# Kernel tuning notes

Hardware: AMD Instinct MI355X
Metric: run time of the kernel (lower is better)

## Reference

```python
import jax, jax.numpy as jnp
import numpy as np
import math

H = 12
DH = 64
MAX_POS = 1024

def setup_inputs() -> dict:
    key = jax.random.key(0)
    ks = jax.random.split(key, 8)
    B, L, D = 2, 1024, 768
    s = 0.02
    return {
        "hidden_states": jax.random.normal(ks[0], (B, L, D), jnp.float32),
        "attention_mask": jnp.zeros((B, 1, 1, L), jnp.float32),
        "struct_matrix": jax.random.uniform(ks[1], (5, B, 1, L, L), jnp.float32),
        "Wq": jax.random.normal(ks[2], (D, D), jnp.float32) * s,
        "bq": jnp.zeros((D,), jnp.float32),
        "Wk": jax.random.normal(ks[3], (D, D), jnp.float32) * s,
        "bk": jnp.zeros((D,), jnp.float32),
        "Wv": jax.random.normal(ks[4], (D, D), jnp.float32) * s,
        "bv": jnp.zeros((D,), jnp.float32),
        "dist_emb": jax.random.normal(ks[5], (2 * MAX_POS - 1, DH), jnp.float32) * s,
        "ssan_w": jax.random.normal(ks[6], (5, H, DH, DH), jnp.float32) * s,
        "abs_bias": jnp.zeros((5, H), jnp.float32),
    }

def reference(hidden_states, attention_mask, struct_matrix, Wq, bq, Wk, bk, Wv, bv, dist_emb, ssan_w, abs_bias):
    B, L, D = hidden_states.shape

    def heads(x):  # [B,L,D] -> [B,H,L,dh]
        return x.reshape(B, L, H, DH).transpose(0, 2, 1, 3)

    q = heads(hidden_states @ Wq + bq)
    k = heads(hidden_states @ Wk + bk)
    v = heads(hidden_states @ Wv + bv)

    scores = jnp.einsum('bhqd,bhkd->bhqk', q, k)

    # relative_key_query positional scores
    pos_ids = jnp.arange(L)
    distance = pos_ids[:, None] - pos_ids[None, :]          # [L,L]
    pos = dist_emb[distance + MAX_POS - 1]                  # [L,L,dh]
    scores = scores + jnp.einsum('bhld,lrd->bhlr', q, pos)
    scores = scores + jnp.einsum('bhrd,lrd->bhlr', k, pos)

    scores = scores / math.sqrt(DH)
    scores = scores + attention_mask

    # 5 SSAN bilinear bias terms, masked by structural matrices
    for i in range(5):
        bias = jnp.einsum('bhqd,hde,bhke->bhqk', q, ssan_w[i], k)
        scores = scores + (bias + abs_bias[i][None, :, None, None]) * struct_matrix[i]

    probs = jax.nn.softmax(scores, axis=-1)
    ctx = jnp.einsum('bhqk,bhkd->bqhd', probs, v).reshape(B, L, D)
    return ctx
```

## Files before the change

kernel.cpp:

```cpp
#include <hip/hip_runtime.h>
#include <math.h>

#define NB 2
#define NL 1024
#define ND 768
#define NH 12
#define DH 64

typedef _Float16 f16;
typedef _Float16 f16x4 __attribute__((ext_vector_type(4)));
typedef _Float16 f16x8 __attribute__((ext_vector_type(8)));
typedef float f32x4 __attribute__((ext_vector_type(4)));

#define MFMA16(a, b, c) __builtin_amdgcn_mfma_f32_16x16x32_f16((a), (b), (c), 0, 0, 0)

__device__ __forceinline__ void soft_barrier() {
    asm volatile("s_waitcnt lgkmcnt(0)\n\ts_barrier" ::: "memory");
}

__global__ __launch_bounds__(256) void prep_kernel(
    const float* __restrict__ hs,
    const float* __restrict__ Wq, const float* __restrict__ Wk,
    const float* __restrict__ Wv, const float* __restrict__ sw,
    const float* __restrict__ de,
    f16* __restrict__ hsf, f16* __restrict__ wt, f16* __restrict__ swt,
    f16* __restrict__ de16)
{
    __shared__ float sT[64 * 66];
    const int t = threadIdx.x;
    const int tile = blockIdx.x;

    if (tile < 768) {
        const int base = tile * 2048 + t * 8;
        float4 a = *(const float4*)&hs[base];
        float4 b = *(const float4*)&hs[base + 4];
        f16x8 hv;
        hv[0] = (f16)a.x; hv[1] = (f16)a.y; hv[2] = (f16)a.z; hv[3] = (f16)a.w;
        hv[4] = (f16)b.x; hv[5] = (f16)b.y; hv[6] = (f16)b.z; hv[7] = (f16)b.w;
        *(f16x8*)&hsf[base] = hv;
        return;
    }
    if (tile >= 1260) {
        const int base = (tile - 1260) * 2048 + t * 8;
        if (base < 2047 * 64) {
            float4 a = *(const float4*)&de[base];
            float4 b = *(const float4*)&de[base + 4];
            f16x8 hv;
            hv[0] = (f16)a.x; hv[1] = (f16)a.y; hv[2] = (f16)a.z; hv[3] = (f16)a.w;
            hv[4] = (f16)b.x; hv[5] = (f16)b.y; hv[6] = (f16)b.z; hv[7] = (f16)b.w;
            *(f16x8*)&de16[base] = hv;
        }
        return;
    }

    const float* S; f16* D; int sRS, dRS;
    const int ti = tile - 768;
    if (ti < 432) {
        const int mat = ti / 144, r2 = ti % 144, ht = r2 / 12, kt = r2 % 12;
        const float* W = (mat == 0) ? Wq : (mat == 1) ? Wk : Wv;
        S = W + (size_t)(kt * 64) * ND + ht * 64;
        D = wt + (size_t)((mat * NH + ht) * 64) * ND + kt * 64;
        sRS = ND; dRS = ND;
    } else {
        const int i = ti - 432;
        S = sw + (size_t)i * 4096;
        D = swt + (size_t)i * 4096;
        sRS = 64; dRS = 64;
    }

    {
        const int kk = t >> 2, nb = (t & 3) * 16;
        float v[16];
        #pragma unroll
        for (int j = 0; j < 4; ++j)
            *(float4*)&v[4 * j] = *(const float4*)&S[(size_t)kk * sRS + nb + 4 * j];
        #pragma unroll
        for (int jj = 0; jj < 16; ++jj)
            sT[(nb + jj) * 66 + kk] = v[jj];
    }
    soft_barrier();
    {
        const int n = t >> 2, kb = (t & 3) * 16;
        f16 tmp[16];
        #pragma unroll
        for (int j = 0; j < 8; ++j) {
            float2 x = *(float2*)&sT[n * 66 + kb + 2 * j];
            tmp[2 * j]     = (f16)x.x;
            tmp[2 * j + 1] = (f16)x.y;
        }
        *(f16x8*)&D[(size_t)n * dRS + kb]     = *(f16x8*)&tmp[0];
        *(f16x8*)&D[(size_t)n * dRS + kb + 8] = *(f16x8*)&tmp[8];
    }
}

__global__ __launch_bounds__(256, 4) void qkv_kernel(
    const f16* __restrict__ hsf, const f16* __restrict__ wt,
    const float* __restrict__ bq, const float* __restrict__ bk,
    const float* __restrict__ bv,
    f16* __restrict__ qf, f16* __restrict__ kf, f16* __restrict__ vt)
{
    __shared__ f16 sA[64 * 72], sB[64 * 72];
    __shared__ float sT[64 * 66];

    const int m0  = blockIdx.x * 64;
    const int y   = blockIdx.y;
    const int mat = y / NH, h = y % NH;
    const int t = threadIdx.x, lane = t & 63, w = t >> 6;
    const int quad = lane >> 4, l15 = lane & 15;
    const int wm = w >> 1, wn = w & 1;

    const float* bias = (mat == 0) ? bq : (mat == 1) ? bk : bv;

    f32x4 acc[2][2];
    #pragma unroll
    for (int r = 0; r < 2; ++r)
        #pragma unroll
        for (int c = 0; c < 2; ++c) acc[r][c] = (f32x4){0.f, 0.f, 0.f, 0.f};

    const int srow = t >> 2, scol = (t & 3) * 16;
    const f16* Ag = hsf + (size_t)(m0 + srow) * ND + scol;
    const f16* Bg = wt + ((size_t)y * 64 + srow) * ND + scol;

    for (int k0 = 0; k0 < ND; k0 += 64) {
        soft_barrier();
        *(f16x8*)&sA[srow * 72 + scol]     = *(const f16x8*)&Ag[k0];
        *(f16x8*)&sA[srow * 72 + scol + 8] = *(const f16x8*)&Ag[k0 + 8];
        *(f16x8*)&sB[srow * 72 + scol]     = *(const f16x8*)&Bg[k0];
        *(f16x8*)&sB[srow * 72 + scol + 8] = *(const f16x8*)&Bg[k0 + 8];
        soft_barrier();
        #pragma unroll
        for (int kk = 0; kk < 64; kk += 32) {
            const int ko = kk + quad * 8;
            f16x8 a0 = *(f16x8*)&sA[(32 * wm + l15) * 72 + ko];
            f16x8 a1 = *(f16x8*)&sA[(32 * wm + 16 + l15) * 72 + ko];
            f16x8 b0 = *(f16x8*)&sB[(32 * wn + l15) * 72 + ko];
            f16x8 b1 = *(f16x8*)&sB[(32 * wn + 16 + l15) * 72 + ko];
            acc[0][0] = MFMA16(a0, b0, acc[0][0]);
            acc[0][1] = MFMA16(a0, b1, acc[0][1]);
            acc[1][0] = MFMA16(a1, b0, acc[1][0]);
            acc[1][1] = MFMA16(a1, b1, acc[1][1]);
        }
    }
    soft_barrier();

    const int bb = m0 >> 10;
    const int lbase = m0 & 1023;
    const int bh = bb * NH + h;

    if (mat < 2) {
        #pragma unroll
        for (int r = 0; r < 2; ++r)
            #pragma unroll
            for (int c = 0; c < 2; ++c) {
                const int col = 32 * wn + 16 * c + l15;
                const float bz = bias[h * 64 + col];
                #pragma unroll
                for (int rr = 0; rr < 4; ++rr)
                    sT[(32 * wm + 16 * r + 4 * quad + rr) * 66 + col] = acc[r][c][rr] + bz;
            }
        soft_barrier();
        const int orow = t >> 2, ocb = (t & 3) * 16;
        f16 tmp[16];
        #pragma unroll
        for (int j = 0; j < 8; ++j) {
            float2 x = *(float2*)&sT[orow * 66 + ocb + 2 * j];
            tmp[2 * j] = (f16)x.x; tmp[2 * j + 1] = (f16)x.y;
        }
        f16* dst = ((mat == 0) ? qf : kf) + ((size_t)bh * NL + lbase + orow) * DH + ocb;
        *(f16x8*)dst       = *(f16x8*)&tmp[0];
        *(f16x8*)(dst + 8) = *(f16x8*)&tmp[8];
    } else {
        #pragma unroll
        for (int r = 0; r < 2; ++r)
            #pragma unroll
            for (int c = 0; c < 2; ++c) {
                const int col = 32 * wn + 16 * c + l15;
                const float bz = bias[h * 64 + col];
                #pragma unroll
                for (int rr = 0; rr < 4; ++rr)
                    sT[col * 66 + 32 * wm + 16 * r + 4 * quad + rr] = acc[r][c][rr] + bz;
            }
        soft_barrier();
        const int d = t >> 2, lcb = (t & 3) * 16;
        f16 tmp[16];
        #pragma unroll
        for (int j = 0; j < 8; ++j) {
            float2 x = *(float2*)&sT[d * 66 + lcb + 2 * j];
            tmp[2 * j] = (f16)x.x; tmp[2 * j + 1] = (f16)x.y;
        }
        f16* dst = vt + ((size_t)bh * DH + d) * NL + lbase + lcb;
        *(f16x8*)dst       = *(f16x8*)&tmp[0];
        *(f16x8*)(dst + 8) = *(f16x8*)&tmp[8];
    }
}

__global__ __launch_bounds__(256, 4) void qw_kernel(
    const f16* __restrict__ qf, const f16* __restrict__ swt,
    f16* __restrict__ qwf)
{
    __shared__ f16 sA[64 * 72], sB[64 * 72];
    __shared__ float sT[64 * 66];

    const int l0 = blockIdx.x * 64;
    const int z  = blockIdx.y;
    const int p  = z / 24, bh = z % 24, h = bh % NH;
    const int t = threadIdx.x, lane = t & 63, w = t >> 6;
    const int quad = lane >> 4, l15 = lane & 15;
    const int wm = w >> 1, wn = w & 1;

    const int srow = t >> 2, scol = (t & 3) * 16;
    {
        const f16* As = qf + ((size_t)bh * NL + l0 + srow) * DH + scol;
        const f16* Bs = swt + ((size_t)(p * NH + h) * 64 + srow) * 64 + scol;
        *(f16x8*)&sA[srow * 72 + scol]     = *(const f16x8*)As;
        *(f16x8*)&sA[srow * 72 + scol + 8] = *(const f16x8*)(As + 8);
        *(f16x8*)&sB[srow * 72 + scol]     = *(const f16x8*)Bs;
        *(f16x8*)&sB[srow * 72 + scol + 8] = *(const f16x8*)(Bs + 8);
    }
    soft_barrier();

    f32x4 acc[2][2];
    #pragma unroll
    for (int r = 0; r < 2; ++r)
        #pragma unroll
        for (int c = 0; c < 2; ++c) acc[r][c] = (f32x4){0.f, 0.f, 0.f, 0.f};

    #pragma unroll
    for (int kk = 0; kk < 64; kk += 32) {
        const int ko = kk + quad * 8;
        f16x8 a0 = *(f16x8*)&sA[(32 * wm + l15) * 72 + ko];
        f16x8 a1 = *(f16x8*)&sA[(32 * wm + 16 + l15) * 72 + ko];
        f16x8 b0 = *(f16x8*)&sB[(32 * wn + l15) * 72 + ko];
        f16x8 b1 = *(f16x8*)&sB[(32 * wn + 16 + l15) * 72 + ko];
        acc[0][0] = MFMA16(a0, b0, acc[0][0]);
        acc[0][1] = MFMA16(a0, b1, acc[0][1]);
        acc[1][0] = MFMA16(a1, b0, acc[1][0]);
        acc[1][1] = MFMA16(a1, b1, acc[1][1]);
    }
    soft_barrier();

    #pragma unroll
    for (int r = 0; r < 2; ++r)
        #pragma unroll
        for (int c = 0; c < 2; ++c) {
            const int col = 32 * wn + 16 * c + l15;
            #pragma unroll
            for (int rr = 0; rr < 4; ++rr)
                sT[(32 * wm + 16 * r + 4 * quad + rr) * 66 + col] = acc[r][c][rr];
        }
    soft_barrier();

    const int orow = t >> 2, ocb = (t & 3) * 16;
    f16 tmp[16];
    #pragma unroll
    for (int j = 0; j < 8; ++j) {
        float2 x = *(float2*)&sT[orow * 66 + ocb + 2 * j];
        tmp[2 * j] = (f16)x.x; tmp[2 * j + 1] = (f16)x.y;
    }
    f16* dst = qwf + ((size_t)(p * 24 + bh) * NL + l0 + orow) * DH + ocb;
    *(f16x8*)dst       = *(f16x8*)&tmp[0];
    *(f16x8*)(dst + 8) = *(f16x8*)&tmp[8];
}

__global__ __launch_bounds__(256, 2) void attn_kernel(
    const f16* __restrict__ qf, const f16* __restrict__ kf,
    const f16* __restrict__ vt, const f16* __restrict__ qwf,
    const float* __restrict__ mask, const float* __restrict__ struct_m,
    const f16* __restrict__ de16, const float* __restrict__ abs_bias,
    float* __restrict__ out)
{
    __shared__ f16 sK[64 * 72];
    __shared__ f16 sVt[2][64 * 72];
    __shared__ f16 sE[96 * 72];
    __shared__ f16 sQEl[96 * 34];
    __shared__ f16 sKEl[96 * 66];
    __shared__ float sS[32 * 68];
    __shared__ f16 sP[32 * 72];
    __shared__ float sAlpha[32], sL[32];

    const int l0 = blockIdx.x * 32;
    const int bh = blockIdx.y;
    const int bb = bh / NH, h = bh % NH;
    const int t  = threadIdx.x;
    const int lane  = t & 63;
    const int w     = t >> 6;
    const int quad  = lane >> 4;
    const int l15   = lane & 15;
    const int msub  = w >> 1;
    const int npair = w & 1;

    const size_t NQKV = (size_t)NB * NH * NL * DH;

    f16x8 aQ[2], aW[5][2];
    {
        const size_t qrow = ((size_t)bh * NL + l0 + 16 * msub + l15) * DH;
        #pragma unroll
        for (int K = 0; K < 2; ++K) {
            aQ[K] = *(const f16x8*)&qf[qrow + 32 * K + 8 * quad];
            #pragma unroll
            for (int p = 0; p < 5; ++p)
                aW[p][K] = *(const f16x8*)&qwf[p * NQKV + qrow + 32 * K + 8 * quad];
        }
    }

    float ab[5];
    #pragma unroll
    for (int p = 0; p < 5; ++p) ab[p] = abs_bias[p * NH + h];

    float pf_st[5][2][4], pf_mask[2];

    auto stage_kv = [&](int r0s, int buf) {
        const int row = t >> 3, col = (t & 7) * 8;
        const f16* ks = kf + ((size_t)bh * NL + r0s) * DH;
        *(f16x8*)&sK[row * 72 + col]        = *(const f16x8*)&ks[row * 64 + col];
        *(f16x8*)&sK[(row + 32) * 72 + col] = *(const f16x8*)&ks[(row + 32) * 64 + col];
        const f16* vs = vt + (size_t)bh * DH * NL + r0s;
        *(f16x8*)&sVt[buf][row * 72 + col] =
            *(const f16x8*)&vs[(size_t)row * NL + col];
        *(f16x8*)&sVt[buf][(row + 32) * 72 + col] =
            *(const f16x8*)&vs[(size_t)(row + 32) * NL + col];
    };

    auto stage_E = [&](int r0s) {
        const int ebase = l0 - r0s + 960;
        #pragma unroll
        for (int p = 0; p < 3; ++p) {
            const int idx = t + 256 * p;
            const int er = idx >> 3, col = (idx & 7) * 8;
            if (er < 95)
                *(f16x8*)&sE[er * 72 + col] =
                    *(const f16x8*)&de16[(size_t)(ebase + er) * DH + col];
        }
    };

    auto prefetch = [&](int r0s) {
        #pragma unroll
        for (int n = 0; n < 2; ++n) {
            const int j = 32 * npair + 16 * n + l15;
            pf_mask[n] = mask[bb * NL + r0s + j];
            #pragma unroll
            for (int r = 0; r < 4; ++r) {
                const int i = 16 * msub + 4 * quad + r;
                #pragma unroll
                for (int p = 0; p < 5; ++p)
                    pf_st[p][n][r] =
                        struct_m[((size_t)(p * NB + bb) * NL + l0 + i) * NL + r0s + j];
            }
        }
    };

    stage_kv(0, 0);
    stage_E(0);
    prefetch(0);

    const int sm_i = t >> 3;
    const int sm_jb = t & 7;
    float m_cur = -INFINITY, l_cur = 0.f;
    f32x4 O[2];
    O[0] = (f32x4){0.f, 0.f, 0.f, 0.f};
    O[1] = (f32x4){0.f, 0.f, 0.f, 0.f};

    for (int kt = 0; kt < 16; ++kt) {
        const int cur = kt & 1;
        soft_barrier();

        {
            f16x8 ak0 = *(f16x8*)&sK[(16 * w + l15) * 72 + quad * 8];
            f16x8 ak1 = *(f16x8*)&sK[(16 * w + l15) * 72 + 32 + quad * 8];
            #pragma unroll
            for (int c = 0; c < 3; ++c) {
                const int nt = 3 * npair + c;
                f16x8 e0 = *(f16x8*)&sE[(16 * nt + l15) * 72 + quad * 8];
                f16x8 e1 = *(f16x8*)&sE[(16 * nt + l15) * 72 + 32 + quad * 8];
                f32x4 cq = {0.f, 0.f, 0.f, 0.f};
                cq = MFMA16(aQ[0], e0, cq);
                cq = MFMA16(aQ[1], e1, cq);
                #pragma unroll
                for (int r = 0; r < 4; ++r)
                    sQEl[(16 * nt + l15) * 34 + 16 * msub + 4 * quad + r] = (f16)cq[r];
            }
            #pragma unroll
            for (int nt = 0; nt < 6; ++nt) {
                f16x8 e0 = *(f16x8*)&sE[(16 * nt + l15) * 72 + quad * 8];
                f16x8 e1 = *(f16x8*)&sE[(16 * nt + l15) * 72 + 32 + quad * 8];
                f32x4 ck = {0.f, 0.f, 0.f, 0.f};
                ck = MFMA16(ak0, e0, ck);
                ck = MFMA16(ak1, e1, ck);
                #pragma unroll
                for (int r = 0; r < 4; ++r)
                    sKEl[(16 * nt + l15) * 66 + 16 * w + 4 * quad + r] = (f16)ck[r];
            }
        }
        soft_barrier();

        {
            f32x4 acc[2][6];
            #pragma unroll
            for (int n = 0; n < 2; ++n)
                #pragma unroll
                for (int p = 0; p < 6; ++p)
                    acc[n][p] = (f32x4){0.f, 0.f, 0.f, 0.f};

            #pragma unroll
            for (int K = 0; K < 2; ++K) {
                const int koff = K * 32 + quad * 8;
                f16x8 bk2[2];
                #pragma unroll
                for (int n = 0; n < 2; ++n)
                    bk2[n] = *(f16x8*)&sK[(32 * npair + 16 * n + l15) * 72 + koff];
                #pragma unroll
                for (int n = 0; n < 2; ++n)
                    acc[n][0] = MFMA16(aQ[K], bk2[n], acc[n][0]);
                #pragma unroll
                for (int p = 0; p < 5; ++p)
                    #pragma unroll
                    for (int n = 0; n < 2; ++n)
                        acc[n][1 + p] = MFMA16(aW[p][K], bk2[n], acc[n][1 + p]);
            }

            #pragma unroll
            for (int n = 0; n < 2; ++n) {
                const int j = 32 * npair + 16 * n + l15;
                #pragma unroll
                for (int r = 0; r < 4; ++r) {
                    const int i = 16 * msub + 4 * quad + r;
                    const int tp = i - j + 63;
                    float posv = (float)sQEl[tp * 34 + i] + (float)sKEl[tp * 66 + j];
                    float s = (acc[n][0][r] + posv) * 0.125f + pf_mask[n];
                    #pragma unroll
                    for (int p = 0; p < 5; ++p)
                        s += (acc[n][1 + p][r] + ab[p]) * pf_st[p][n][r];
                    sS[i * 68 + j] = s;
                }
            }
        }
        soft_barrier();

        {
            float sv[8];
            float smax = -INFINITY;
            #pragma unroll
            for (int k = 0; k < 8; ++k) {
                sv[k] = sS[sm_i * 68 + sm_jb + 8 * k];
                smax = fmaxf(smax, sv[k]);
            }
            #pragma unroll
            for (int off = 4; off > 0; off >>= 1)
                smax = fmaxf(smax, __shfl_xor(smax, off, 8));
            const float m_new = fmaxf(m_cur, smax);
            const float alpha = __expf(m_cur - m_new);
            float rsum = 0.f;
            #pragma unroll
            for (int k = 0; k < 8; ++k) {
                float p = __expf(sv[k] - m_new);
                sP[sm_i * 72 + sm_jb + 8 * k] = (f16)p;
                rsum += p;
            }
            #pragma unroll
            for (int off = 4; off > 0; off >>= 1)
                rsum += __shfl_xor(rsum, off, 8);
            l_cur = l_cur * alpha + rsum;
            m_cur = m_new;
            if (sm_jb == 0) { sAlpha[sm_i] = alpha; sL[sm_i] = l_cur; }
        }
        soft_barrier();

        {
            if (kt < 15) {
                stage_kv((kt + 1) * 64, cur ^ 1);
                stage_E((kt + 1) * 64);
                prefetch((kt + 1) * 64);
            }

            float a4[4];
            #pragma unroll
            for (int r = 0; r < 4; ++r) a4[r] = sAlpha[16 * msub + 4 * quad + r];
            #pragma unroll
            for (int n = 0; n < 2; ++n)
                #pragma unroll
                for (int r = 0; r < 4; ++r) O[n][r] *= a4[r];

            const int prow = (16 * msub + l15) * 72;
            #pragma unroll
            for (int K = 0; K < 2; ++K) {
                const int koff = K * 32 + quad * 8;
                f16x8 pfr = *(f16x8*)&sP[prow + koff];
                #pragma unroll
                for (int n = 0; n < 2; ++n) {
                    f16x8 vfr = *(f16x8*)&sVt[cur][(32 * npair + 16 * n + l15) * 72 + koff];
                    O[n] = MFMA16(pfr, vfr, O[n]);
                }
            }
        }
    }

    float linv[4];
    #pragma unroll
    for (int r = 0; r < 4; ++r) linv[r] = 1.0f / sL[16 * msub + 4 * quad + r];
    #pragma unroll
    for (int n = 0; n < 2; ++n) {
        const int dh = 32 * npair + 16 * n + l15;
        #pragma unroll
        for (int r = 0; r < 4; ++r) {
            const int i = 16 * msub + 4 * quad + r;
            out[((size_t)bb * NL + l0 + i) * ND + h * DH + dh] = O[n][r] * linv[r];
        }
    }
}

extern "C" void kernel_launch(void* const* d_in, const int* in_sizes, int n_in,
                              void* d_out, int out_size, void* d_ws, size_t ws_size,
                              hipStream_t stream) {
    const float* hs   = (const float*)d_in[0];
    const float* mask = (const float*)d_in[1];
    const float* stm  = (const float*)d_in[2];
    const float* Wq   = (const float*)d_in[3];
    const float* bq   = (const float*)d_in[4];
    const float* Wk   = (const float*)d_in[5];
    const float* bk   = (const float*)d_in[6];
    const float* Wv   = (const float*)d_in[7];
    const float* bv   = (const float*)d_in[8];
    const float* de   = (const float*)d_in[9];
    const float* sw   = (const float*)d_in[10];
    const float* abb  = (const float*)d_in[11];
    float* outp = (float*)d_out;

    const size_t NQKV = (size_t)NB * NH * NL * DH;
    char* ws = (char*)d_ws;
    f16* qf   = (f16*)ws;                 ws += NQKV * 2;
    f16* kf   = (f16*)ws;                 ws += NQKV * 2;
    f16* vtb  = (f16*)ws;                 ws += NQKV * 2;
    f16* qwf  = (f16*)ws;                 ws += 5 * NQKV * 2;
    f16* hsf  = (f16*)ws;                 ws += NQKV * 2;
    f16* wt   = (f16*)ws;                 ws += (size_t)2304 * 768 * 2;
    f16* swt  = (f16*)ws;                 ws += (size_t)245760 * 2;
    f16* de16 = (f16*)ws;

    prep_kernel<<<1324, 256, 0, stream>>>(hs, Wq, Wk, Wv, sw, de,
                                          hsf, wt, swt, de16);
    qkv_kernel<<<dim3(32, 36), 256, 0, stream>>>(hsf, wt, bq, bk, bv, qf, kf, vtb);
    qw_kernel<<<dim3(16, 120), 256, 0, stream>>>(qf, swt, qwf);
    attn_kernel<<<dim3(32, 24), 256, 0, stream>>>(qf, kf, vtb, qwf,
                                                  mask, stm, de16, abb, outp);
}
```

Before: 243.2 us.

## Fold SSAN weights into Q projection and widen attention to 512 threads

Precomputes Wq·ssan_w[i] per head, plus the matching projected bias, in a new small kernel. The five qW projections then come directly from hidden_states inside one merged projection GEMM, which removes the separate qw kernel and its serial dependency on q. The attention kernel moves from 256 to 512 threads, with each wave owning one 16-column tile, and the relative-position Q/K·E products are redistributed across all waves with a reshaped shared layout. The qW GEMM now has a K dimension of 768 instead of 64, so it does more FLOPs, and the product is folded in fp16, which may change accuracy slightly.

```diff
diff --git a/kernel.cpp b/kernel.cpp
--- a/kernel.cpp
+++ b/kernel.cpp
@@ -21,10 +21,8 @@
 __global__ __launch_bounds__(256) void prep_kernel(
     const float* __restrict__ hs,
     const float* __restrict__ Wq, const float* __restrict__ Wk,
-    const float* __restrict__ Wv, const float* __restrict__ sw,
-    const float* __restrict__ de,
-    f16* __restrict__ hsf, f16* __restrict__ wt, f16* __restrict__ swt,
-    f16* __restrict__ de16)
+    const float* __restrict__ Wv, const float* __restrict__ de,
+    f16* __restrict__ hsf, f16* __restrict__ wt, f16* __restrict__ de16)
 {
     __shared__ float sT[64 * 66];
     const int t = threadIdx.x;
@@ -40,8 +38,8 @@
         *(f16x8*)&hsf[base] = hv;
         return;
     }
-    if (tile >= 1260) {
-        const int base = (tile - 1260) * 2048 + t * 8;
+    if (tile >= 1200) {
+        const int base = (tile - 1200) * 2048 + t * 8;
         if (base < 2047 * 64) {
             float4 a = *(const float4*)&de[base];
             float4 b = *(const float4*)&de[base + 4];
@@ -53,27 +51,18 @@
         return;
     }
 
-    const float* S; f16* D; int sRS, dRS;
     const int ti = tile - 768;
-    if (ti < 432) {
-        const int mat = ti / 144, r2 = ti % 144, ht = r2 / 12, kt = r2 % 12;
-        const float* W = (mat == 0) ? Wq : (mat == 1) ? Wk : Wv;
-        S = W + (size_t)(kt * 64) * ND + ht * 64;
-        D = wt + (size_t)((mat * NH + ht) * 64) * ND + kt * 64;
-        sRS = ND; dRS = ND;
-    } else {
-        const int i = ti - 432;
-        S = sw + (size_t)i * 4096;
-        D = swt + (size_t)i * 4096;
-        sRS = 64; dRS = 64;
-    }
+    const int mat = ti / 144, r2 = ti % 144, ht = r2 / 12, kt = r2 % 12;
+    const float* W = (mat == 0) ? Wq : (mat == 1) ? Wk : Wv;
+    const float* S = W + (size_t)(kt * 64) * ND + ht * 64;
+    f16* D = wt + (size_t)((mat * NH + ht) * 64) * ND + kt * 64;
 
     {
         const int kk = t >> 2, nb = (t & 3) * 16;
         float v[16];
         #pragma unroll
         for (int j = 0; j < 4; ++j)
-            *(float4*)&v[4 * j] = *(const float4*)&S[(size_t)kk * sRS + nb + 4 * j];
+            *(float4*)&v[4 * j] = *(const float4*)&S[(size_t)kk * ND + nb + 4 * j];
         #pragma unroll
         for (int jj = 0; jj < 16; ++jj)
             sT[(nb + jj) * 66 + kk] = v[jj];
@@ -88,23 +77,102 @@
             tmp[2 * j]     = (f16)x.x;
             tmp[2 * j + 1] = (f16)x.y;
         }
-        *(f16x8*)&D[(size_t)n * dRS + kb]     = *(f16x8*)&tmp[0];
-        *(f16x8*)&D[(size_t)n * dRS + kb + 8] = *(f16x8*)&tmp[8];
+        *(f16x8*)&D[(size_t)n * ND + kb]     = *(f16x8*)&tmp[0];
+        *(f16x8*)&D[(size_t)n * ND + kb + 8] = *(f16x8*)&tmp[8];
     }
 }
 
-__global__ __launch_bounds__(256, 4) void qkv_kernel(
+__global__ __launch_bounds__(256, 2) void wq5_kernel(
+    const float* __restrict__ Wq, const float* __restrict__ bq,
+    const float* __restrict__ sw,
+    f16* __restrict__ wq5t, float* __restrict__ bq5)
+{
+    __shared__ float sAT[64 * 69];
+    __shared__ float sB[64 * 64];
+    __shared__ float sT[64 * 66];
+
+    const int ktile = blockIdx.x;
+    const int z  = blockIdx.y;
+    const int h  = z % NH;
+    const int k0 = ktile * 64;
+    const int t  = threadIdx.x;
+
+    {
+        const int kk = t >> 2, db = (t & 3) * 16;
+        float v[16];
+        #pragma unroll
+        for (int j = 0; j < 4; ++j)
+            *(float4*)&v[4 * j] = *(const float4*)&Wq[(size_t)(k0 + kk) * ND + h * 64 + db + 4 * j];
+        #pragma unroll
+        for (int jj = 0; jj < 16; ++jj)
+            sAT[(db + jj) * 69 + kk] = v[jj];
+        #pragma unroll
+        for (int j = 0; j < 4; ++j)
+            *(float4*)&sB[16 * t + 4 * j] = *(const float4*)&sw[(size_t)z * 4096 + 16 * t + 4 * j];
+    }
+    soft_barrier();
+
+    const int tr = t >> 4, tc = t & 15;
+    float acc[4][4];
+    #pragma unroll
+    for (int r = 0; r < 4; ++r)
+        #pragma unroll
+        for (int c = 0; c < 4; ++c) acc[r][c] = 0.f;
+
+    #pragma unroll 8
+    for (int d = 0; d < 64; ++d) {
+        float a[4], b[4];
+        *(float4*)a = *(const float4*)&sAT[d * 69 + tr * 4];
+        *(float4*)b = *(const float4*)&sB[d * 64 + tc * 4];
+        #pragma unroll
+        for (int r = 0; r < 4; ++r)
+            #pragma unroll
+            for (int c = 0; c < 4; ++c)
+                acc[r][c] += a[r] * b[c];
+    }
+
+    if (ktile == 0 && t < 64) {
+        float s = 0.f;
+        for (int d = 0; d < 64; ++d) s += bq[h * 64 + d] * sB[d * 64 + t];
+        bq5[z * 64 + t] = s;
+    }
+
+    #pragma unroll
+    for (int r = 0; r < 4; ++r)
+        #pragma unroll
+        for (int c = 0; c < 4; ++c)
+            sT[(tc * 4 + c) * 66 + tr * 4 + r] = acc[r][c];
+    soft_barrier();
+
+    const int e = t >> 2, kb = (t & 3) * 16;
+    f16 tmp[16];
+    #pragma unroll
+    for (int j = 0; j < 8; ++j) {
+        float2 x = *(float2*)&sT[e * 66 + kb + 2 * j];
+        tmp[2 * j] = (f16)x.x; tmp[2 * j + 1] = (f16)x.y;
+    }
+    f16* dst = wq5t + ((size_t)z * 64 + e) * ND + k0 + kb;
+    *(f16x8*)dst       = *(f16x8*)&tmp[0];
+    *(f16x8*)(dst + 8) = *(f16x8*)&tmp[8];
+}
+
+__global__ __launch_bounds__(256, 4) void proj_kernel(
     const f16* __restrict__ hsf, const f16* __restrict__ wt,
+    const f16* __restrict__ wq5t, const float* __restrict__ bq5,
     const float* __restrict__ bq, const float* __restrict__ bk,
     const float* __restrict__ bv,
-    f16* __restrict__ qf, f16* __restrict__ kf, f16* __restrict__ vt)
+    f16* __restrict__ qf, f16* __restrict__ kf, f16* __restrict__ vt,
+    f16* __restrict__ qwf)
 {
     __shared__ f16 sA[64 * 72], sB[64 * 72];
     __shared__ float sT[64 * 66];
 
     const int m0  = blockIdx.x * 64;
     const int y   = blockIdx.y;
-    const int mat = y / NH, h = y % NH;
+    const bool isqw = (y >= 36);
+    const int mat = isqw ? 3 : y / NH;
+    const int z2  = isqw ? (y - 36) : 0;
+    const int h   = isqw ? (z2 % NH) : (y % NH);
     const int t = threadIdx.x, lane = t & 63, w = t >> 6;
     const int quad = lane >> 4, l15 = lane & 15;
     const int wm = w >> 1, wn = w & 1;
@@ -119,7 +187,8 @@
 
     const int srow = t >> 2, scol = (t & 3) * 16;
     const f16* Ag = hsf + (size_t)(m0 + srow) * ND + scol;
-    const f16* Bg = wt + ((size_t)y * 64 + srow) * ND + scol;
+    const f16* Bg = (isqw ? wq5t + (size_t)z2 * 64 * ND : wt + (size_t)y * 64 * ND)
+                    + (size_t)srow * ND + scol;
 
     for (int k0 = 0; k0 < ND; k0 += 64) {
         soft_barrier();
@@ -147,29 +216,7 @@
     const int lbase = m0 & 1023;
     const int bh = bb * NH + h;
 
-    if (mat < 2) {
-        #pragma unroll
-        for (int r = 0; r < 2; ++r)
-            #pragma unroll
-            for (int c = 0; c < 2; ++c) {
-                const int col = 32 * wn + 16 * c + l15;
-                const float bz = bias[h * 64 + col];
-                #pragma unroll
-                for (int rr = 0; rr < 4; ++rr)
-                    sT[(32 * wm + 16 * r + 4 * quad + rr) * 66 + col] = acc[r][c][rr] + bz;
-            }
-        soft_barrier();
-        const int orow = t >> 2, ocb = (t & 3) * 16;
-        f16 tmp[16];
-        #pragma unroll
-        for (int j = 0; j < 8; ++j) {
-            float2 x = *(float2*)&sT[orow * 66 + ocb + 2 * j];
-            tmp[2 * j] = (f16)x.x; tmp[2 * j + 1] = (f16)x.y;
-        }
-        f16* dst = ((mat == 0) ? qf : kf) + ((size_t)bh * NL + lbase + orow) * DH + ocb;
-        *(f16x8*)dst       = *(f16x8*)&tmp[0];
-        *(f16x8*)(dst + 8) = *(f16x8*)&tmp[8];
-    } else {
+    if (mat == 2) {
         #pragma unroll
         for (int r = 0; r < 2; ++r)
             #pragma unroll
@@ -191,89 +238,50 @@
         f16* dst = vt + ((size_t)bh * DH + d) * NL + lbase + lcb;
         *(f16x8*)dst       = *(f16x8*)&tmp[0];
         *(f16x8*)(dst + 8) = *(f16x8*)&tmp[8];
+    } else {
+        #pragma unroll
+        for (int r = 0; r < 2; ++r)
+            #pragma unroll
+            for (int c = 0; c < 2; ++c) {
+                const int col = 32 * wn + 16 * c + l15;
+                const float bz = isqw ? bq5[z2 * 64 + col] : bias[h * 64 + col];
+                #pragma unroll
+                for (int rr = 0; rr < 4; ++rr)
+                    sT[(32 * wm + 16 * r + 4 * quad + rr) * 66 + col] = acc[r][c][rr] + bz;
+            }
+        soft_barrier();
+        const int orow = t >> 2, ocb = (t & 3) * 16;
+        f16 tmp[16];
+        #pragma unroll
+        for (int j = 0; j < 8; ++j) {
+            float2 x = *(float2*)&sT[orow * 66 + ocb + 2 * j];
+            tmp[2 * j] = (f16)x.x; tmp[2 * j + 1] = (f16)x.y;
+        }
+        f16* dst;
+        if (isqw) {
+            const int p = z2 / NH;
+            dst = qwf + ((size_t)(p * 24 + bh) * NL + lbase + orow) * DH + ocb;
+        } else {
+            dst = ((mat == 0) ? qf : kf) + ((size_t)bh * NL + lbase + orow) * DH + ocb;
+        }
+        *(f16x8*)dst       = *(f16x8*)&tmp[0];
+        *(f16x8*)(dst + 8) = *(f16x8*)&tmp[8];
     }
 }
 
-__global__ __launch_bounds__(256, 4) void qw_kernel(
-    const f16* __restrict__ qf, const f16* __restrict__ swt,
-    f16* __restrict__ qwf)
-{
-    __shared__ f16 sA[64 * 72], sB[64 * 72];
-    __shared__ float sT[64 * 66];
-
-    const int l0 = blockIdx.x * 64;
-    const int z  = blockIdx.y;
-    const int p  = z / 24, bh = z % 24, h = bh % NH;
-    const int t = threadIdx.x, lane = t & 63, w = t >> 6;
-    const int quad = lane >> 4, l15 = lane & 15;
-    const int wm = w >> 1, wn = w & 1;
-
-    const int srow = t >> 2, scol = (t & 3) * 16;
-    {
-        const f16* As = qf + ((size_t)bh * NL + l0 + srow) * DH + scol;
-        const f16* Bs = swt + ((size_t)(p * NH + h) * 64 + srow) * 64 + scol;
-        *(f16x8*)&sA[srow * 72 + scol]     = *(const f16x8*)As;
-        *(f16x8*)&sA[srow * 72 + scol + 8] = *(const f16x8*)(As + 8);
-        *(f16x8*)&sB[srow * 72 + scol]     = *(const f16x8*)Bs;
-        *(f16x8*)&sB[srow * 72 + scol + 8] = *(const f16x8*)(Bs + 8);
-    }
-    soft_barrier();
-
-    f32x4 acc[2][2];
-    #pragma unroll
-    for (int r = 0; r < 2; ++r)
-        #pragma unroll
-        for (int c = 0; c < 2; ++c) acc[r][c] = (f32x4){0.f, 0.f, 0.f, 0.f};
-
-    #pragma unroll
-    for (int kk = 0; kk < 64; kk += 32) {
-        const int ko = kk + quad * 8;
-        f16x8 a0 = *(f16x8*)&sA[(32 * wm + l15) * 72 + ko];
-        f16x8 a1 = *(f16x8*)&sA[(32 * wm + 16 + l15) * 72 + ko];
-        f16x8 b0 = *(f16x8*)&sB[(32 * wn + l15) * 72 + ko];
-        f16x8 b1 = *(f16x8*)&sB[(32 * wn + 16 + l15) * 72 + ko];
-        acc[0][0] = MFMA16(a0, b0, acc[0][0]);
-        acc[0][1] = MFMA16(a0, b1, acc[0][1]);
-        acc[1][0] = MFMA16(a1, b0, acc[1][0]);
-        acc[1][1] = MFMA16(a1, b1, acc[1][1]);
-    }
-    soft_barrier();
-
-    #pragma unroll
-    for (int r = 0; r < 2; ++r)
-        #pragma unroll
-        for (int c = 0; c < 2; ++c) {
-            const int col = 32 * wn + 16 * c + l15;
-            #pragma unroll
-            for (int rr = 0; rr < 4; ++rr)
-                sT[(32 * wm + 16 * r + 4 * quad + rr) * 66 + col] = acc[r][c][rr];
-        }
-    soft_barrier();
-
-    const int orow = t >> 2, ocb = (t & 3) * 16;
-    f16 tmp[16];
-    #pragma unroll
-    for (int j = 0; j < 8; ++j) {
-        float2 x = *(float2*)&sT[orow * 66 + ocb + 2 * j];
-        tmp[2 * j] = (f16)x.x; tmp[2 * j + 1] = (f16)x.y;
-    }
-    f16* dst = qwf + ((size_t)(p * 24 + bh) * NL + l0 + orow) * DH + ocb;
-    *(f16x8*)dst       = *(f16x8*)&tmp[0];
-    *(f16x8*)(dst + 8) = *(f16x8*)&tmp[8];
-}
-
-__global__ __launch_bounds__(256, 2) void attn_kernel(
+__global__ __launch_bounds__(512, 4) void attn_kernel(
     const f16* __restrict__ qf, const f16* __restrict__ kf,
     const f16* __restrict__ vt, const f16* __restrict__ qwf,
     const float* __restrict__ mask, const float* __restrict__ struct_m,
     const f16* __restrict__ de16, const float* __restrict__ abs_bias,
     float* __restrict__ out)
 {
+    __shared__ f16 sQ[32 * 72];
     __shared__ f16 sK[64 * 72];
     __shared__ f16 sVt[2][64 * 72];
     __shared__ f16 sE[96 * 72];
-    __shared__ f16 sQEl[96 * 34];
-    __shared__ f16 sKEl[96 * 66];
+    __shared__ f16 sQEl[32 * 100];
+    __shared__ f16 sKEl[64 * 100];
     __shared__ float sS[32 * 68];
     __shared__ f16 sP[32 * 72];
     __shared__ float sAlpha[32], sL[32];
@@ -282,12 +290,12 @@
     const int bh = blockIdx.y;
     const int bb = bh / NH, h = bh % NH;
     const int t  = threadIdx.x;
-    const int lane  = t & 63;
-    const int w     = t >> 6;
-    const int quad  = lane >> 4;
-    const int l15   = lane & 15;
-    const int msub  = w >> 1;
-    const int npair = w & 1;
+    const int lane = t & 63;
+    const int w    = t >> 6;
+    const int quad = lane >> 4;
+    const int l15  = lane & 15;
+    const int msub = w >> 2;
+    const int ncol = w & 3;
 
     const size_t NQKV = (size_t)NB * NH * NL * DH;
 
@@ -302,50 +310,46 @@
                 aW[p][K] = *(const f16x8*)&qwf[p * NQKV + qrow + 32 * K + 8 * quad];
         }
     }
+    if (t < 256) {
+        const int row = t >> 3, col = (t & 7) * 8;
+        *(f16x8*)&sQ[row * 72 + col] =
+            *(const f16x8*)&qf[((size_t)bh * NL + l0 + row) * DH + col];
+    }
 
     float ab[5];
     #pragma unroll
     for (int p = 0; p < 5; ++p) ab[p] = abs_bias[p * NH + h];
 
-    float pf_st[5][2][4], pf_mask[2];
+    float pf_st[5][4], pf_mask;
 
     auto stage_kv = [&](int r0s, int buf) {
         const int row = t >> 3, col = (t & 7) * 8;
-        const f16* ks = kf + ((size_t)bh * NL + r0s) * DH;
-        *(f16x8*)&sK[row * 72 + col]        = *(const f16x8*)&ks[row * 64 + col];
-        *(f16x8*)&sK[(row + 32) * 72 + col] = *(const f16x8*)&ks[(row + 32) * 64 + col];
-        const f16* vs = vt + (size_t)bh * DH * NL + r0s;
+        *(f16x8*)&sK[row * 72 + col] =
+            *(const f16x8*)&kf[((size_t)bh * NL + r0s + row) * DH + col];
         *(f16x8*)&sVt[buf][row * 72 + col] =
-            *(const f16x8*)&vs[(size_t)row * NL + col];
-        *(f16x8*)&sVt[buf][(row + 32) * 72 + col] =
-            *(const f16x8*)&vs[(size_t)(row + 32) * NL + col];
+            *(const f16x8*)&vt[((size_t)bh * DH + row) * NL + r0s + col];
     };
-
     auto stage_E = [&](int r0s) {
         const int ebase = l0 - r0s + 960;
         #pragma unroll
-        for (int p = 0; p < 3; ++p) {
-            const int idx = t + 256 * p;
+        for (int p2 = 0; p2 < 2; ++p2) {
+            const int idx = t + 512 * p2;
             const int er = idx >> 3, col = (idx & 7) * 8;
             if (er < 95)
                 *(f16x8*)&sE[er * 72 + col] =
                     *(const f16x8*)&de16[(size_t)(ebase + er) * DH + col];
         }
     };
-
     auto prefetch = [&](int r0s) {
-        #pragma unroll
-        for (int n = 0; n < 2; ++n) {
-            const int j = 32 * npair + 16 * n + l15;
-            pf_mask[n] = mask[bb * NL + r0s + j];
-            #pragma unroll
-            for (int r = 0; r < 4; ++r) {
-                const int i = 16 * msub + 4 * quad + r;
-                #pragma unroll
-                for (int p = 0; p < 5; ++p)
-                    pf_st[p][n][r] =
-                        struct_m[((size_t)(p * NB + bb) * NL + l0 + i) * NL + r0s + j];
-            }
+        const int j = 16 * ncol + l15;
+        pf_mask = mask[bb * NL + r0s + j];
+        #pragma unroll
+        for (int r = 0; r < 4; ++r) {
+            const int i = 16 * msub + 4 * quad + r;
+            #pragma unroll
+            for (int p = 0; p < 5; ++p)
+                pf_st[p][r] =
+                    struct_m[((size_t)(p * NB + bb) * NL + l0 + i) * NL + r0s + j];
         }
     };
 
@@ -353,115 +357,95 @@
     stage_E(0);
     prefetch(0);
 
-    const int sm_i = t >> 3;
-    const int sm_jb = t & 7;
+    const int sm_i = t >> 4;
+    const int sm_c = t & 15;
     float m_cur = -INFINITY, l_cur = 0.f;
-    f32x4 O[2];
-    O[0] = (f32x4){0.f, 0.f, 0.f, 0.f};
-    O[1] = (f32x4){0.f, 0.f, 0.f, 0.f};
+    f32x4 O = (f32x4){0.f, 0.f, 0.f, 0.f};
 
     for (int kt = 0; kt < 16; ++kt) {
         const int cur = kt & 1;
         soft_barrier();
 
-        {
-            f16x8 ak0 = *(f16x8*)&sK[(16 * w + l15) * 72 + quad * 8];
-            f16x8 ak1 = *(f16x8*)&sK[(16 * w + l15) * 72 + 32 + quad * 8];
-            #pragma unroll
-            for (int c = 0; c < 3; ++c) {
-                const int nt = 3 * npair + c;
+        #pragma unroll
+        for (int c = 0; c < 5; ++c) {
+            const int tid = c * 8 + w;
+            if (tid < 36) {
+                const bool isq = (tid < 12);
+                const int u  = isq ? tid : tid - 12;
+                const int rt = u / 6;
+                const int nt = u % 6;
+                const f16* abase = isq ? &sQ[(16 * rt + l15) * 72]
+                                       : &sK[(16 * rt + l15) * 72];
+                f16x8 a0 = *(f16x8*)&abase[quad * 8];
+                f16x8 a1 = *(f16x8*)&abase[32 + quad * 8];
                 f16x8 e0 = *(f16x8*)&sE[(16 * nt + l15) * 72 + quad * 8];
                 f16x8 e1 = *(f16x8*)&sE[(16 * nt + l15) * 72 + 32 + quad * 8];
-                f32x4 cq = {0.f, 0.f, 0.f, 0.f};
-                cq = MFMA16(aQ[0], e0, cq);
-                cq = MFMA16(aQ[1], e1, cq);
+                f32x4 cq = (f32x4){0.f, 0.f, 0.f, 0.f};
+                cq = MFMA16(a0, e0, cq);
+                cq = MFMA16(a1, e1, cq);
+                f16* dstp = isq ? sQEl : sKEl;
+                const int row0 = 16 * rt + 4 * quad;
                 #pragma unroll
                 for (int r = 0; r < 4; ++r)
-                    sQEl[(16 * nt + l15) * 34 + 16 * msub + 4 * quad + r] = (f16)cq[r];
-            }
-            #pragma unroll
-            for (int nt = 0; nt < 6; ++nt) {
-                f16x8 e0 = *(f16x8*)&sE[(16 * nt + l15) * 72 + quad * 8];
-                f16x8 e1 = *(f16x8*)&sE[(16 * nt + l15) * 72 + 32 + quad * 8];
-                f32x4 ck = {0.f, 0.f, 0.f, 0.f};
-                ck = MFMA16(ak0, e0, ck);
-                ck = MFMA16(ak1, e1, ck);
-                #pragma unroll
-                for (int r = 0; r < 4; ++r)
-                    sKEl[(16 * nt + l15) * 66 + 16 * w + 4 * quad + r] = (f16)ck[r];
+                    dstp[(row0 + r) * 100 + 16 * nt + l15] = (f16)cq[r];
             }
         }
         soft_barrier();
 
         {
-            f32x4 acc[2][6];
-            #pragma unroll
-            for (int n = 0; n < 2; ++n)
-                #pragma unroll
-                for (int p = 0; p < 6; ++p)
-                    acc[n][p] = (f32x4){0.f, 0.f, 0.f, 0.f};
-
+            f32x4 acc[6];
+            #pragma unroll
+            for (int p = 0; p < 6; ++p) acc[p] = (f32x4){0.f, 0.f, 0.f, 0.f};
             #pragma unroll
             for (int K = 0; K < 2; ++K) {
                 const int koff = K * 32 + quad * 8;
-                f16x8 bk2[2];
-                #pragma unroll
-                for (int n = 0; n < 2; ++n)
-                    bk2[n] = *(f16x8*)&sK[(32 * npair + 16 * n + l15) * 72 + koff];
-                #pragma unroll
-                for (int n = 0; n < 2; ++n)
-                    acc[n][0] = MFMA16(aQ[K], bk2[n], acc[n][0]);
+                f16x8 bk2 = *(f16x8*)&sK[(16 * ncol + l15) * 72 + koff];
+                acc[0] = MFMA16(aQ[K], bk2, acc[0]);
                 #pragma unroll
                 for (int p = 0; p < 5; ++p)
-                    #pragma unroll
-                    for (int n = 0; n < 2; ++n)
-                        acc[n][1 + p] = MFMA16(aW[p][K], bk2[n], acc[n][1 + p]);
-            }
-
-            #pragma unroll
-            for (int n = 0; n < 2; ++n) {
-                const int j = 32 * npair + 16 * n + l15;
+                    acc[1 + p] = MFMA16(aW[p][K], bk2, acc[1 + p]);
+            }
+            const int j = 16 * ncol + l15;
+            #pragma unroll
+            for (int r = 0; r < 4; ++r) {
+                const int i = 16 * msub + 4 * quad + r;
+                const int tp = i - j + 63;
+                float posv = (float)sQEl[i * 100 + tp] + (float)sKEl[j * 100 + tp];
+                float s = (acc[0][r] + posv) * 0.125f + pf_mask;
                 #pragma unroll
-                for (int r = 0; r < 4; ++r) {
-                    const int i = 16 * msub + 4 * quad + r;
-                    const int tp = i - j + 63;
-                    float posv = (float)sQEl[tp * 34 + i] + (float)sKEl[tp * 66 + j];
-                    float s = (acc[n][0][r] + posv) * 0.125f + pf_mask[n];
-                    #pragma unroll
-                    for (int p = 0; p < 5; ++p)
-                        s += (acc[n][1 + p][r] + ab[p]) * pf_st[p][n][r];
-                    sS[i * 68 + j] = s;
-                }
+                for (int p = 0; p < 5; ++p)
+                    s += (acc[1 + p][r] + ab[p]) * pf_st[p][r];
+                sS[i * 68 + j] = s;
             }
         }
         soft_barrier();
 
         {
-            float sv[8];
+            float sv[4];
             float smax = -INFINITY;
             #pragma unroll
-            for (int k = 0; k < 8; ++k) {
-                sv[k] = sS[sm_i * 68 + sm_jb + 8 * k];
+            for (int k = 0; k < 4; ++k) {
+                sv[k] = sS[sm_i * 68 + sm_c + 16 * k];
                 smax = fmaxf(smax, sv[k]);
             }
             #pragma unroll
-            for (int off = 4; off > 0; off >>= 1)
-                smax = fmaxf(smax, __shfl_xor(smax, off, 8));
+            for (int off = 8; off > 0; off >>= 1)
+                smax = fmaxf(smax, __shfl_xor(smax, off, 16));
             const float m_new = fmaxf(m_cur, smax);
             const float alpha = __expf(m_cur - m_new);
             float rsum = 0.f;
             #pragma unroll
-            for (int k = 0; k < 8; ++k) {
+            for (int k = 0; k < 4; ++k) {
                 float p = __expf(sv[k] - m_new);
-                sP[sm_i * 72 + sm_jb + 8 * k] = (f16)p;
+                sP[sm_i * 72 + sm_c + 16 * k] = (f16)p;
                 rsum += p;
             }
             #pragma unroll
-            for (int off = 4; off > 0; off >>= 1)
-                rsum += __shfl_xor(rsum, off, 8);
+            for (int off = 8; off > 0; off >>= 1)
+                rsum += __shfl_xor(rsum, off, 16);
             l_cur = l_cur * alpha + rsum;
             m_cur = m_new;
-            if (sm_jb == 0) { sAlpha[sm_i] = alpha; sL[sm_i] = l_cur; }
+            if (sm_c == 0) { sAlpha[sm_i] = alpha; sL[sm_i] = l_cur; }
         }
         soft_barrier();
 
@@ -471,25 +455,18 @@
                 stage_E((kt + 1) * 64);
                 prefetch((kt + 1) * 64);
             }
-
             float a4[4];
             #pragma unroll
             for (int r = 0; r < 4; ++r) a4[r] = sAlpha[16 * msub + 4 * quad + r];
             #pragma unroll
-            for (int n = 0; n < 2; ++n)
-                #pragma unroll
-                for (int r = 0; r < 4; ++r) O[n][r] *= a4[r];
-
-            const int prow = (16 * msub + l15) * 72;
+            for (int r = 0; r < 4; ++r) O[r] *= a4[r];
+
             #pragma unroll
             for (int K = 0; K < 2; ++K) {
                 const int koff = K * 32 + quad * 8;
-                f16x8 pfr = *(f16x8*)&sP[prow + koff];
-                #pragma unroll
-                for (int n = 0; n < 2; ++n) {
-                    f16x8 vfr = *(f16x8*)&sVt[cur][(32 * npair + 16 * n + l15) * 72 + koff];
-                    O[n] = MFMA16(pfr, vfr, O[n]);
-                }
+                f16x8 pfr = *(f16x8*)&sP[(16 * msub + l15) * 72 + koff];
+                f16x8 vfr = *(f16x8*)&sVt[cur][(16 * ncol + l15) * 72 + koff];
+                O = MFMA16(pfr, vfr, O);
             }
         }
     }
@@ -497,14 +474,11 @@
     float linv[4];
     #pragma unroll
     for (int r = 0; r < 4; ++r) linv[r] = 1.0f / sL[16 * msub + 4 * quad + r];
-    #pragma unroll
-    for (int n = 0; n < 2; ++n) {
-        const int dh = 32 * npair + 16 * n + l15;
-        #pragma unroll
-        for (int r = 0; r < 4; ++r) {
-            const int i = 16 * msub + 4 * quad + r;
-            out[((size_t)bb * NL + l0 + i) * ND + h * DH + dh] = O[n][r] * linv[r];
-        }
+    const int dh = 16 * ncol + l15;
+    #pragma unroll
+    for (int r = 0; r < 4; ++r) {
+        const int i = 16 * msub + 4 * quad + r;
+        out[((size_t)bb * NL + l0 + i) * ND + h * DH + dh] = O[r] * linv[r];
     }
 }
 
@@ -527,19 +501,20 @@
 
     const size_t NQKV = (size_t)NB * NH * NL * DH;
     char* ws = (char*)d_ws;
-    f16* qf   = (f16*)ws;                 ws += NQKV * 2;
-    f16* kf   = (f16*)ws;                 ws += NQKV * 2;
-    f16* vtb  = (f16*)ws;                 ws += NQKV * 2;
-    f16* qwf  = (f16*)ws;                 ws += 5 * NQKV * 2;
-    f16* hsf  = (f16*)ws;                 ws += NQKV * 2;
-    f16* wt   = (f16*)ws;                 ws += (size_t)2304 * 768 * 2;
-    f16* swt  = (f16*)ws;                 ws += (size_t)245760 * 2;
-    f16* de16 = (f16*)ws;
-
-    prep_kernel<<<1324, 256, 0, stream>>>(hs, Wq, Wk, Wv, sw, de,
-                                          hsf, wt, swt, de16);
-    qkv_kernel<<<dim3(32, 36), 256, 0, stream>>>(hsf, wt, bq, bk, bv, qf, kf, vtb);
-    qw_kernel<<<dim3(16, 120), 256, 0, stream>>>(qf, swt, qwf);
-    attn_kernel<<<dim3(32, 24), 256, 0, stream>>>(qf, kf, vtb, qwf,
+    f16*   qf   = (f16*)ws;               ws += NQKV * 2;
+    f16*   kf   = (f16*)ws;               ws += NQKV * 2;
+    f16*   vtb  = (f16*)ws;               ws += NQKV * 2;
+    f16*   qwf  = (f16*)ws;               ws += 5 * NQKV * 2;
+    f16*   hsf  = (f16*)ws;               ws += NQKV * 2;
+    f16*   wt   = (f16*)ws;               ws += (size_t)2304 * 768 * 2;
+    f16*   wq5t = (f16*)ws;               ws += (size_t)60 * 64 * 768 * 2;
+    float* bq5  = (float*)ws;             ws += 3840 * 4;
+    f16*   de16 = (f16*)ws;
+
+    prep_kernel<<<1264, 256, 0, stream>>>(hs, Wq, Wk, Wv, de, hsf, wt, de16);
+    wq5_kernel<<<dim3(12, 60), 256, 0, stream>>>(Wq, bq, sw, wq5t, bq5);
+    proj_kernel<<<dim3(32, 96), 256, 0, stream>>>(hsf, wt, wq5t, bq5,
+                                                  bq, bk, bv, qf, kf, vtb, qwf);
+    attn_kernel<<<dim3(32, 24), 512, 0, stream>>>(qf, kf, vtb, qwf,
                                                   mask, stm, de16, abb, outp);
 }
```

After: 429.3 us. 1.77x slower.
